# Optimization experiments

Hardware: AMD Instinct MI355X
Metric: run time of the kernel (lower is better)

## Reference

```python
import jax, jax.numpy as jnp
import numpy as np


def _conv(x, w, b, pad):
    # x: (B,C,H,W), w: (O,I,kh,kw), NCHW conv with given padding
    y = jax.lax.conv_general_dilated(x, w, window_strides=(1, 1), padding=pad,
                                     dimension_numbers=('NCHW', 'OIHW', 'NCHW'))
    return y + b[None, :, None, None]


def _frn(x, eps):
    # FilterResponseNorm: normalize by rms over spatial dims (2,3)
    nu2 = jnp.mean(x * x, axis=(2, 3), keepdims=True)
    return x * jax.lax.rsqrt(nu2 + jnp.abs(eps))


def _mish(x):
    return x * jnp.tanh(jax.nn.softplus(x))


def setup_inputs() -> dict:
    key = jax.random.key(0)
    ks = jax.random.split(key, 9)
    B, C, H, W = 4, 256, 64, 64
    C16 = C // 16
    x = jax.random.normal(ks[0], (B, C, H, W), dtype=jnp.float32)
    s = 0.05
    wq = jax.random.normal(ks[1], (C16, C, 1, 3), dtype=jnp.float32) * s
    bq = jax.random.normal(ks[2], (C16,), dtype=jnp.float32) * s
    wk = jax.random.normal(ks[3], (C16, C, 3, 1), dtype=jnp.float32) * s
    bk = jax.random.normal(ks[4], (C16,), dtype=jnp.float32) * s
    wv = jax.random.normal(ks[5], (C, C, 1, 1), dtype=jnp.float32) * s
    bv = jax.random.normal(ks[6], (C,), dtype=jnp.float32) * s
    gamma = jax.random.normal(ks[7], (1,), dtype=jnp.float32) * 0.1
    eps_q = jnp.full((1, C16, 1, 1), 1e-6, dtype=jnp.float32)
    eps_k = jnp.full((1, C16, 1, 1), 1e-6, dtype=jnp.float32)
    return {"x": x, "wq": wq, "bq": bq, "wk": wk, "bk": bk,
            "wv": wv, "bv": bv, "gamma": gamma, "eps_q": eps_q, "eps_k": eps_k}


def reference(x, wq, bq, wk, bk, wv, bv, gamma, eps_q, eps_k):
    B, C, H, W = x.shape
    N = H * W
    # query branch: Conv2d(k=(1,3), pad=(0,1)) -> FRN -> Mish
    q = _mish(_frn(_conv(x, wq, bq, [(0, 0), (1, 1)]), eps_q))  # (B,C16,H,W)
    # key branch: Conv2d(k=(3,1), pad=(1,0)) -> FRN -> Mish
    k = _mish(_frn(_conv(x, wk, bk, [(1, 1), (0, 0)]), eps_k))  # (B,C16,H,W)
    q = q.reshape(B, -1, N)  # (B,C16,N)
    k = k.reshape(B, -1, N)  # (B,C16,N)
    # affinity[b,n,m] = sum_c q[b,c,n] * k[b,c,m]; softmax over m
    affinity = jnp.einsum('bcn,bcm->bnm', q, k)
    affinity = jax.nn.softmax(affinity, axis=-1)  # (B,N,N)
    v = _conv(x, wv, bv, [(0, 0), (0, 0)]).reshape(B, C, N)  # (B,C,N)
    # weights = v @ affinity^T : weights[b,c,j] = sum_n v[b,c,n] * affinity[b,j,n]
    weights = jnp.einsum('bcn,bjn->bcj', v, affinity).reshape(B, C, H, W)
    return gamma * weights + x
```

## Files before the change

kernel.cpp:

```cpp
#include <hip/hip_runtime.h>
#include <stdint.h>

#define NB 4
#define CC 256
#define C16 16
#define HH 64
#define WW 64
#define NN 4096

typedef __attribute__((ext_vector_type(8))) short short8;
typedef __attribute__((ext_vector_type(4))) float floatx4;
typedef __attribute__((ext_vector_type(16))) float floatx16;

#if __has_builtin(__builtin_amdgcn_exp2f)
#define EXP2(x) __builtin_amdgcn_exp2f(x)
#else
#define EXP2(x) exp2f(x)
#endif

__device__ __forceinline__ unsigned short f2bf(float f) {
    union { float f; unsigned u; } v; v.f = f;
    unsigned r = v.u + 0x7fffu + ((v.u >> 16) & 1u);
    return (unsigned short)(r >> 16);
}
__device__ __forceinline__ float bf2f(unsigned short h) {
    union { unsigned u; float f; } v; v.u = (unsigned)h << 16;
    return v.f;
}


__global__ __launch_bounds__(256) void prep_kernel(
        const float* __restrict__ x, const float* __restrict__ wv,
        const float* __restrict__ wq, const float* __restrict__ wk,
        unsigned short* __restrict__ xT, unsigned short* __restrict__ wvb,
        unsigned short* __restrict__ wqkb, float* __restrict__ nu2) {
    int bid = blockIdx.x;
    if (bid < 1024) {
        __shared__ float tile_t[64][65];
        int nt = bid & 63, ct = (bid >> 6) & 3, b = bid >> 8;
        int n0 = nt * 64, c0 = ct * 64;
        int tid = threadIdx.x;
        int rg = tid >> 4, f = tid & 15;
        const float* xb = x + ((size_t)b * CC + c0) * NN + n0;
#pragma unroll
        for (int p = 0; p < 4; ++p) {
            int c = p * 16 + rg;
            float4 v = *(const float4*)(xb + (size_t)c * NN + f * 4);
            tile_t[f * 4 + 0][c] = v.x;
            tile_t[f * 4 + 1][c] = v.y;
            tile_t[f * 4 + 2][c] = v.z;
            tile_t[f * 4 + 3][c] = v.w;
        }
        __syncthreads();
        unsigned short* xtb = xT + ((size_t)b * NN + n0) * CC + c0;
#pragma unroll
        for (int p = 0; p < 4; ++p) {
            int n = p * 16 + rg;
            ushort4 st;
            st.x = f2bf(tile_t[n][f * 4 + 0]);
            st.y = f2bf(tile_t[n][f * 4 + 1]);
            st.z = f2bf(tile_t[n][f * 4 + 2]);
            st.w = f2bf(tile_t[n][f * 4 + 3]);
            *(ushort4*)(xtb + (size_t)n * CC + f * 4) = st;
        }
    } else {
        int idx = (bid - 1024) * 256 + threadIdx.x;
        if (bid == 1024 && threadIdx.x < 128) nu2[threadIdx.x] = 0.f;
        if (idx < 16384) {
            float4 v = *(const float4*)(wv + idx * 4);
            ushort4 o;
            o.x = f2bf(v.x); o.y = f2bf(v.y); o.z = f2bf(v.z); o.w = f2bf(v.w);
            *(ushort4*)(wvb + idx * 4) = o;
        } else if (idx < 16384 + 6144) {
            int base = (idx - 16384) * 4;
#pragma unroll
            for (int u = 0; u < 4; ++u) {
                int e = base + u;
                int t = e / 12288;
                int i = e - t * 12288;
                int tap = i >> 12, o = (i >> 8) & 15, c = i & 255;
                const float* src = t ? wk : wq;
                wqkb[e] = f2bf(src[o * 768 + c * 3 + tap]);
            }
        }
    }
}

__global__ __launch_bounds__(256) void conv_kernel(
        const unsigned short* __restrict__ xT, const unsigned short* __restrict__ wvb,
        const unsigned short* __restrict__ wqkb, const float* __restrict__ bv,
        const float* __restrict__ bq, const float* __restrict__ bk,
        unsigned short* __restrict__ vb, unsigned short* __restrict__ qrawh,
        unsigned short* __restrict__ krawh, float* __restrict__ nu2) {
    int bid = blockIdx.x;
    int tid = threadIdx.x;
    int wv_ = tid >> 6, lane = tid & 63;
    int q16 = lane >> 4, c16 = lane & 15;
    if (bid < 512) {
        int ntile = bid & 63, b = (bid >> 6) & 3, ch = bid >> 8;
        int n0 = ntile * 64;
        int cb = ch * 128 + wv_ * 32;
        floatx4 fzero = {0.f, 0.f, 0.f, 0.f};
        floatx4 acc[2][4];
        for (int ct = 0; ct < 2; ++ct)
            for (int nt = 0; nt < 4; ++nt) acc[ct][nt] = fzero;
        const unsigned short* xb = xT + ((size_t)b * NN + n0) * CC;
        for (int kc = 0; kc < 8; ++kc) {
            int ko = kc * 32 + q16 * 8;
            short8 a0 = *(const short8*)(wvb + (size_t)(cb + c16) * CC + ko);
            short8 a1 = *(const short8*)(wvb + (size_t)(cb + 16 + c16) * CC + ko);
            short8 bf[4];
#pragma unroll
            for (int nt = 0; nt < 4; ++nt)
                bf[nt] = *(const short8*)(xb + (size_t)(nt * 16 + c16) * CC + ko);
#pragma unroll
            for (int nt = 0; nt < 4; ++nt) {
                acc[0][nt] = __builtin_amdgcn_mfma_f32_16x16x32_bf16(bf[nt], a0, acc[0][nt], 0, 0, 0);
                acc[1][nt] = __builtin_amdgcn_mfma_f32_16x16x32_bf16(bf[nt], a1, acc[1][nt], 0, 0, 0);
            }
        }
        float bv0 = bv[cb + c16], bv1 = bv[cb + 16 + c16];
        int off = 32 * 8 * (q16 >> 1) + (q16 & 1) * 4 + c16 * 8;
#pragma unroll
        for (int ct = 0; ct < 2; ++ct) {
            float bvv = ct ? bv1 : bv0;
#pragma unroll
            for (int nt = 0; nt < 4; ++nt) {
                size_t fb = (((size_t)b * 8 + ch * 4 + wv_) * 256 + (n0 >> 4) + nt) * 512;
                ushort4 st;
                st.x = f2bf(acc[ct][nt][0] + bvv);
                st.y = f2bf(acc[ct][nt][1] + bvv);
                st.z = f2bf(acc[ct][nt][2] + bvv);
                st.w = f2bf(acc[ct][nt][3] + bvv);
                *(ushort4*)(vb + fb + off + ct * 16 * 8) = st;
            }
        }
    } else {
        int cv = bid - 512;
        int nb2 = cv & 63, b = cv >> 6;
        int nl = nb2 * 64 + wv_ * 16 + c16;
        int h = nl >> 6, w = nl & 63;
        bool vm1 = (w != 0), vp1 = (w != 63);
        bool vm64 = (h != 0), vp64 = (h != 63);
        short8 zero8 = {0, 0, 0, 0, 0, 0, 0, 0};
        floatx4 accq = {0.f, 0.f, 0.f, 0.f}, acck = {0.f, 0.f, 0.f, 0.f};
        const unsigned short* xb = xT + (size_t)b * NN * CC;
        const unsigned short* wrow = wqkb + c16 * 256;
        for (int kc = 0; kc < 8; ++kc) {
            int ko = kc * 32 + q16 * 8;
            short8 b0 = *(const short8*)(xb + (size_t)nl * CC + ko);
            short8 bm1 = vm1 ? *(const short8*)(xb + (size_t)(nl - 1) * CC + ko) : zero8;
            short8 bp1 = vp1 ? *(const short8*)(xb + (size_t)(nl + 1) * CC + ko) : zero8;
            short8 bm64 = vm64 ? *(const short8*)(xb + (size_t)(nl - 64) * CC + ko) : zero8;
            short8 bp64 = vp64 ? *(const short8*)(xb + (size_t)(nl + 64) * CC + ko) : zero8;
            short8 aq0 = *(const short8*)(wrow + 0 * 4096 + ko);
            short8 aq1 = *(const short8*)(wrow + 1 * 4096 + ko);
            short8 aq2 = *(const short8*)(wrow + 2 * 4096 + ko);
            short8 ak0 = *(const short8*)(wrow + 12288 + 0 * 4096 + ko);
            short8 ak1 = *(const short8*)(wrow + 12288 + 1 * 4096 + ko);
            short8 ak2 = *(const short8*)(wrow + 12288 + 2 * 4096 + ko);
            accq = __builtin_amdgcn_mfma_f32_16x16x32_bf16(bm1, aq0, accq, 0, 0, 0);
            accq = __builtin_amdgcn_mfma_f32_16x16x32_bf16(b0, aq1, accq, 0, 0, 0);
            accq = __builtin_amdgcn_mfma_f32_16x16x32_bf16(bp1, aq2, accq, 0, 0, 0);
            acck = __builtin_amdgcn_mfma_f32_16x16x32_bf16(bm64, ak0, acck, 0, 0, 0);
            acck = __builtin_amdgcn_mfma_f32_16x16x32_bf16(b0, ak1, acck, 0, 0, 0);
            acck = __builtin_amdgcn_mfma_f32_16x16x32_bf16(bp64, ak2, acck, 0, 0, 0);
        }
        int nst = nb2 * 64 + wv_ * 16 + q16 * 4;
        float bqv = bq[c16], bkv = bk[c16];
        ushort4 sq4, sk4;
        float ssq = 0.f, ssk = 0.f;
        {
            float vq0 = accq[0] + bqv, vq1 = accq[1] + bqv, vq2 = accq[2] + bqv, vq3 = accq[3] + bqv;
            float vk0 = acck[0] + bkv, vk1 = acck[1] + bkv, vk2 = acck[2] + bkv, vk3 = acck[3] + bkv;
            sq4.x = f2bf(vq0); sq4.y = f2bf(vq1); sq4.z = f2bf(vq2); sq4.w = f2bf(vq3);
            sk4.x = f2bf(vk0); sk4.y = f2bf(vk1); sk4.z = f2bf(vk2); sk4.w = f2bf(vk3);
            ssq = vq0 * vq0 + vq1 * vq1 + vq2 * vq2 + vq3 * vq3;
            ssk = vk0 * vk0 + vk1 * vk1 + vk2 * vk2 + vk3 * vk3;
        }
        *(ushort4*)(qrawh + (size_t)(b * C16 + c16) * NN + nst) = sq4;
        *(ushort4*)(krawh + (size_t)(b * C16 + c16) * NN + nst) = sk4;
        ssq += __shfl_xor(ssq, 16, 64);
        ssq += __shfl_xor(ssq, 32, 64);
        ssk += __shfl_xor(ssk, 16, 64);
        ssk += __shfl_xor(ssk, 32, 64);
        if (lane < 16) {
            atomicAdd(nu2 + b * C16 + lane, ssq);
            atomicAdd(nu2 + 64 + b * C16 + lane, ssk);
        }
    }
}

__global__ __launch_bounds__(256) void frn_mish_kernel(
        const unsigned short* __restrict__ qrawh, const unsigned short* __restrict__ krawh,
        const float* __restrict__ nu2, const float* __restrict__ eps_q,
        const float* __restrict__ eps_k, unsigned short* __restrict__ qb,
        unsigned short* __restrict__ kb) {
    int blk = blockIdx.x;
    int tensor = blk >> 8;
    int b = (blk >> 6) & 3;
    int nch = blk & 63;
    const unsigned short* raw = tensor ? krawh : qrawh;
    const float* eps = tensor ? eps_k : eps_q;
    unsigned short* outp = tensor ? kb : qb;
    const float* nu = nu2 + tensor * 64 + b * C16;
    float scale = tensor ? 1.0f : 1.44269504f;
    int n = nch * 64 + (threadIdx.x & 63);
    int oq = threadIdx.x >> 6;
    ushort4 pk4;
#pragma unroll
    for (int i = 0; i < 4; ++i) {
        int o = oq * 4 + i;
        float r = bf2f(raw[(size_t)(b * C16 + o) * NN + n]);
        float v = r * rsqrtf(nu[o] * (1.f / (float)NN) + fabsf(eps[o]));
        float sp = fmaxf(v, 0.f) + log1pf(expf(-fabsf(v)));
        float m = v * tanhf(sp) * scale;
        ((unsigned short*)&pk4)[i] = f2bf(m);
    }
    size_t base = ((size_t)b * 128 + (n >> 5)) * 512 + (size_t)(n & 31) * 8
                + (size_t)(oq >> 1) * 256 + (oq & 1) * 4;
    *(ushort4*)(outp + base) = pk4;
}

__device__ __forceinline__ void pack_half(
        const floatx16& sc, int h, short8* A, float* lsum) {
    unsigned pk[4];
    float ls = 0.f;
#pragma unroll
    for (int p = 0; p < 4; ++p) {
        float e0 = EXP2(sc[8 * h + 2 * p]);
        float e1 = EXP2(sc[8 * h + 2 * p + 1]);
        ls += e0 + e1;
        pk[p] = __builtin_amdgcn_perm(__float_as_uint(e1), __float_as_uint(e0), 0x07060302u);
    }
    *lsum += ls;
    asm("v_permlane32_swap_b32 %0, %1" : "+v"(pk[0]), "+v"(pk[2]));
    asm("v_permlane32_swap_b32 %0, %1" : "+v"(pk[1]), "+v"(pk[3]));
    union { unsigned u[4]; short8 s; } a;
    a.u[0] = pk[0]; a.u[1] = pk[1]; a.u[2] = pk[2]; a.u[3] = pk[3];
    *A = a.s;
}

__global__ __launch_bounds__(256, 2) void attn_kernel(
        const unsigned short* __restrict__ qb, const unsigned short* __restrict__ kb,
        const unsigned short* __restrict__ vb, const float* __restrict__ x,
        const float* __restrict__ gamma_p, float* __restrict__ out) {
    __shared__ float lpart[4][2][32];
    __shared__ float obuf[4][32][33];

    int tid = threadIdx.x;
    int wv_ = __builtin_amdgcn_readfirstlane(tid >> 6);
    int lane = tid & 63;
    int l31 = lane & 31, lh = lane >> 5;
    int id = blockIdx.x;
    int cs = id & 1, b = (id >> 1) & 3, jt = id >> 3;
    int jbase = jt * 64, cb = cs * 128;
    int lane8 = lane * 8;

    const unsigned short* qfb = qb + ((size_t)b * 128 + (jbase >> 5)) * 512 + lane8;
    const unsigned short* kfb = kb + ((size_t)b * 128 + (wv_ * 32)) * 512 + lane8;

    short8 qf0 = *(const short8*)qfb;
    short8 qf1 = *(const short8*)(qfb + 512);

    floatx16 z16 = {0,0,0,0,0,0,0,0,0,0,0,0,0,0,0,0};
    floatx16 acc0[4], acc1[4];
#pragma unroll
    for (int cg = 0; cg < 4; ++cg) { acc0[cg] = z16; acc1[cg] = z16; }
    float lsum0 = 0.f, lsum1 = 0.f;

    const unsigned short* vp0 = vb + (((size_t)b * 8 + cs * 4 + 0) * 256 + wv_ * 64) * 512 + lane8;
    const unsigned short* vp1 = vb + (((size_t)b * 8 + cs * 4 + 1) * 256 + wv_ * 64) * 512 + lane8;
    const unsigned short* vp2 = vb + (((size_t)b * 8 + cs * 4 + 2) * 256 + wv_ * 64) * 512 + lane8;
    const unsigned short* vp3 = vb + (((size_t)b * 8 + cs * 4 + 3) * 256 + wv_ * 64) * 512 + lane8;

    short8 ak = *(const short8*)kfb;
#pragma unroll 1
    for (int step = 0; step < 32; ++step) {
        short8 vf0a = *(const short8*)vp0;
        short8 vf1a = *(const short8*)vp1;
        short8 vf2a = *(const short8*)vp2;
        short8 vf3a = *(const short8*)vp3;
        short8 vf0b = *(const short8*)(vp0 + 512);
        short8 vf1b = *(const short8*)(vp1 + 512);
        short8 vf2b = *(const short8*)(vp2 + 512);
        short8 vf3b = *(const short8*)(vp3 + 512);
        floatx16 sc0 = __builtin_amdgcn_mfma_f32_32x32x16_bf16(ak, qf0, z16, 0, 0, 0);
        floatx16 sc1 = __builtin_amdgcn_mfma_f32_32x32x16_bf16(ak, qf1, z16, 0, 0, 0);
        ak = *(const short8*)(kfb + (size_t)((step + 1) & 31) * 512);
        short8 A;
        pack_half(sc0, 0, &A, &lsum0);
        __builtin_amdgcn_s_setprio(1);
        acc0[0] = __builtin_amdgcn_mfma_f32_32x32x16_bf16(A, vf0a, acc0[0], 0, 0, 0);
        acc0[1] = __builtin_amdgcn_mfma_f32_32x32x16_bf16(A, vf1a, acc0[1], 0, 0, 0);
        acc0[2] = __builtin_amdgcn_mfma_f32_32x32x16_bf16(A, vf2a, acc0[2], 0, 0, 0);
        acc0[3] = __builtin_amdgcn_mfma_f32_32x32x16_bf16(A, vf3a, acc0[3], 0, 0, 0);
        __builtin_amdgcn_s_setprio(0);
        __builtin_amdgcn_sched_barrier(0);
        pack_half(sc0, 1, &A, &lsum0);
        __builtin_amdgcn_s_setprio(1);
        acc0[0] = __builtin_amdgcn_mfma_f32_32x32x16_bf16(A, vf0b, acc0[0], 0, 0, 0);
        acc0[1] = __builtin_amdgcn_mfma_f32_32x32x16_bf16(A, vf1b, acc0[1], 0, 0, 0);
        acc0[2] = __builtin_amdgcn_mfma_f32_32x32x16_bf16(A, vf2b, acc0[2], 0, 0, 0);
        acc0[3] = __builtin_amdgcn_mfma_f32_32x32x16_bf16(A, vf3b, acc0[3], 0, 0, 0);
        __builtin_amdgcn_s_setprio(0);
        __builtin_amdgcn_sched_barrier(0);
        pack_half(sc1, 0, &A, &lsum1);
        __builtin_amdgcn_s_setprio(1);
        acc1[0] = __builtin_amdgcn_mfma_f32_32x32x16_bf16(A, vf0a, acc1[0], 0, 0, 0);
        acc1[1] = __builtin_amdgcn_mfma_f32_32x32x16_bf16(A, vf1a, acc1[1], 0, 0, 0);
        acc1[2] = __builtin_amdgcn_mfma_f32_32x32x16_bf16(A, vf2a, acc1[2], 0, 0, 0);
        acc1[3] = __builtin_amdgcn_mfma_f32_32x32x16_bf16(A, vf3a, acc1[3], 0, 0, 0);
        __builtin_amdgcn_s_setprio(0);
        __builtin_amdgcn_sched_barrier(0);
        pack_half(sc1, 1, &A, &lsum1);
        __builtin_amdgcn_s_setprio(1);
        acc1[0] = __builtin_amdgcn_mfma_f32_32x32x16_bf16(A, vf0b, acc1[0], 0, 0, 0);
        acc1[1] = __builtin_amdgcn_mfma_f32_32x32x16_bf16(A, vf1b, acc1[1], 0, 0, 0);
        acc1[2] = __builtin_amdgcn_mfma_f32_32x32x16_bf16(A, vf2b, acc1[2], 0, 0, 0);
        acc1[3] = __builtin_amdgcn_mfma_f32_32x32x16_bf16(A, vf3b, acc1[3], 0, 0, 0);
        __builtin_amdgcn_s_setprio(0);
        vp0 += 1024; vp1 += 1024; vp2 += 1024; vp3 += 1024;
    }

    lsum0 += __shfl_xor(lsum0, 32, 64);
    lsum1 += __shfl_xor(lsum1, 32, 64);
    if (lh == 0) { lpart[wv_][0][l31] = lsum0; lpart[wv_][1][l31] = lsum1; }
    __syncthreads();

    int j31 = tid & 31;
    float gamma = gamma_p[0];
    float gl0 = gamma / (lpart[0][0][j31] + lpart[1][0][j31] + lpart[2][0][j31] + lpart[3][0][j31]);
    float gl1 = gamma / (lpart[0][1][j31] + lpart[1][1][j31] + lpart[2][1][j31] + lpart[3][1][j31]);
    const float* xbb = x + (size_t)b * CC * NN;
    float* obb = out + (size_t)b * CC * NN;
    int hofs = lh * 4;
    int cgrp = tid >> 5;
#pragma unroll
    for (int jg = 0; jg < 2; ++jg) {
        float gl = jg ? gl1 : gl0;
#pragma unroll
        for (int cg = 0; cg < 4; ++cg) {
            __syncthreads();
            const floatx16& a = jg ? acc1[cg] : acc0[cg];
#pragma unroll
            for (int r = 0; r < 16; ++r) {
                int row = (r & 3) + 8 * (r >> 2) + hofs;
                obuf[wv_][row][l31] = a[r];
            }
            __syncthreads();
#pragma unroll
            for (int i = 0; i < 4; ++i) {
                int c = cgrp * 4 + i;
                float val = obuf[0][j31][c] + obuf[1][j31][c] + obuf[2][j31][c] + obuf[3][j31][c];
                size_t oidx = (size_t)(cb + cg * 32 + c) * NN + jbase + jg * 32 + j31;
                obb[oidx] = fmaf(gl, val, xbb[oidx]);
            }
        }
    }
}

extern "C" void kernel_launch(void* const* d_in, const int* in_sizes, int n_in,
                              void* d_out, int out_size, void* d_ws, size_t ws_size,
                              hipStream_t stream) {
    const float* x     = (const float*)d_in[0];
    const float* wq    = (const float*)d_in[1];
    const float* bq    = (const float*)d_in[2];
    const float* wk    = (const float*)d_in[3];
    const float* bk    = (const float*)d_in[4];
    const float* wv    = (const float*)d_in[5];
    const float* bv    = (const float*)d_in[6];
    const float* gamma = (const float*)d_in[7];
    const float* eps_q = (const float*)d_in[8];
    const float* eps_k = (const float*)d_in[9];
    float* out = (float*)d_out;

    char* ws = (char*)d_ws;
    unsigned short* qrawh = (unsigned short*)ws;
    unsigned short* krawh = (unsigned short*)(ws + (1u << 20));
    float* nu2  = (float*)(ws + (2u << 20));
    unsigned short* qb = (unsigned short*)(ws + (2u << 20) + 4096);
    unsigned short* kb = qb + (size_t)NB * NN * C16;
    unsigned short* vb = kb + (size_t)NB * NN * C16;
    unsigned short* xT = vb + (size_t)NB * CC * NN;
    unsigned short* wvb = xT + (size_t)NB * NN * CC;
    unsigned short* wqkb = wvb + (size_t)CC * CC;

    prep_kernel<<<dim3(1112), dim3(256), 0, stream>>>(x, wv, wq, wk, xT, wvb, wqkb, nu2);
    conv_kernel<<<dim3(768), dim3(256), 0, stream>>>(xT, wvb, wqkb, bv, bq, bk, vb, qrawh, krawh, nu2);
    frn_mish_kernel<<<dim3(512), dim3(256), 0, stream>>>(qrawh, krawh, nu2, eps_q, eps_k, qb, kb);
    attn_kernel<<<dim3(512), dim3(256), 0, stream>>>(qb, kb, vb, x, gamma, out);
}
```

Baseline: 163.3 us.

## Double-buffer V fragments through LDS with async global_load_lds prefetch

The V operand loads in the attention main loop no longer go straight from global memory into registers. They are now issued as asynchronous global-to-LDS loads into per-wave double buffers one step ahead, then read back from LDS after an explicit vmcnt wait. The goal is to hide global-memory latency behind the MFMA and exp work of the current step. In exchange LDS use grows to about 66 KB per block, and the output staging buffer now aliases the stage buffers. The final prefetch reads one step past the end of each V slice.

```diff
diff --git a/kernel.cpp b/kernel.cpp
--- a/kernel.cpp
+++ b/kernel.cpp
@@ -26,6 +26,12 @@
 __device__ __forceinline__ float bf2f(unsigned short h) {
     union { unsigned u; float f; } v; v.u = (unsigned)h << 16;
     return v.f;
+}
+
+__device__ __forceinline__ void gll16(const unsigned short* g, char* l) {
+    __builtin_amdgcn_global_load_lds(
+        (const __attribute__((address_space(1))) void*)g,
+        (__attribute__((address_space(3))) void*)l, 16, 0, 0);
 }
 
 
@@ -245,8 +251,9 @@
         const unsigned short* __restrict__ qb, const unsigned short* __restrict__ kb,
         const unsigned short* __restrict__ vb, const float* __restrict__ x,
         const float* __restrict__ gamma_p, float* __restrict__ out) {
-    __shared__ float lpart[4][2][32];
-    __shared__ float obuf[4][32][33];
+    __shared__ __align__(1024) char smem[66560];
+    float (*lpart)[2][32] = (float (*)[2][32])(smem + 65536);
+    float (*obuf)[32][33] = (float (*)[32][33])smem;
 
     int tid = threadIdx.x;
     int wv_ = __builtin_amdgcn_readfirstlane(tid >> 6);
@@ -256,6 +263,10 @@
     int cs = id & 1, b = (id >> 1) & 3, jt = id >> 3;
     int jbase = jt * 64, cb = cs * 128;
     int lane8 = lane * 8;
+    int lane16 = lane * 16;
+
+    char* st0 = smem + wv_ * 8192;
+    char* st1 = st0 + 32768;
 
     const unsigned short* qfb = qb + ((size_t)b * 128 + (jbase >> 5)) * 512 + lane8;
     const unsigned short* kfb = kb + ((size_t)b * 128 + (wv_ * 32)) * 512 + lane8;
@@ -274,54 +285,84 @@
     const unsigned short* vp2 = vb + (((size_t)b * 8 + cs * 4 + 2) * 256 + wv_ * 64) * 512 + lane8;
     const unsigned short* vp3 = vb + (((size_t)b * 8 + cs * 4 + 3) * 256 + wv_ * 64) * 512 + lane8;
 
-    short8 ak = *(const short8*)kfb;
+#define STAGE8(WRB) do { \
+        gll16(vp0,       (WRB) + 0 * 1024); \
+        gll16(vp1,       (WRB) + 1 * 1024); \
+        gll16(vp2,       (WRB) + 2 * 1024); \
+        gll16(vp3,       (WRB) + 3 * 1024); \
+        gll16(vp0 + 512, (WRB) + 4 * 1024); \
+        gll16(vp1 + 512, (WRB) + 5 * 1024); \
+        gll16(vp2 + 512, (WRB) + 6 * 1024); \
+        gll16(vp3 + 512, (WRB) + 7 * 1024); \
+        vp0 += 1024; vp1 += 1024; vp2 += 1024; vp3 += 1024; \
+    } while (0)
+
+    STAGE8(st0);
+    short8 ak0 = *(const short8*)kfb;
+    short8 ak1;
+    int kstep = 1;
+
+#define STEP(RDB, WRB, AKC, AKN) do { \
+        STAGE8(WRB); \
+        AKN = *(const short8*)(kfb + (size_t)(kstep & 31) * 512); ++kstep; \
+        __builtin_amdgcn_sched_barrier(0); \
+        asm volatile("s_waitcnt vmcnt(10)" ::: "memory"); \
+        __builtin_amdgcn_sched_barrier(0); \
+        short8 vf0a = *(const short8*)((RDB) + 0 * 1024 + lane16); \
+        short8 vf1a = *(const short8*)((RDB) + 1 * 1024 + lane16); \
+        short8 vf2a = *(const short8*)((RDB) + 2 * 1024 + lane16); \
+        short8 vf3a = *(const short8*)((RDB) + 3 * 1024 + lane16); \
+        short8 vf0b = *(const short8*)((RDB) + 4 * 1024 + lane16); \
+        short8 vf1b = *(const short8*)((RDB) + 5 * 1024 + lane16); \
+        short8 vf2b = *(const short8*)((RDB) + 6 * 1024 + lane16); \
+        short8 vf3b = *(const short8*)((RDB) + 7 * 1024 + lane16); \
+        floatx16 sc0 = __builtin_amdgcn_mfma_f32_32x32x16_bf16(AKC, qf0, z16, 0, 0, 0); \
+        floatx16 sc1 = __builtin_amdgcn_mfma_f32_32x32x16_bf16(AKC, qf1, z16, 0, 0, 0); \
+        short8 A; \
+        pack_half(sc0, 0, &A, &lsum0); \
+        __builtin_amdgcn_s_setprio(1); \
+        acc0[0] = __builtin_amdgcn_mfma_f32_32x32x16_bf16(A, vf0a, acc0[0], 0, 0, 0); \
+        acc0[1] = __builtin_amdgcn_mfma_f32_32x32x16_bf16(A, vf1a, acc0[1], 0, 0, 0); \
+        acc0[2] = __builtin_amdgcn_mfma_f32_32x32x16_bf16(A, vf2a, acc0[2], 0, 0, 0); \
+        acc0[3] = __builtin_amdgcn_mfma_f32_32x32x16_bf16(A, vf3a, acc0[3], 0, 0, 0); \
+        __builtin_amdgcn_s_setprio(0); \
+        __builtin_amdgcn_sched_barrier(0); \
+        pack_half(sc0, 1, &A, &lsum0); \
+        __builtin_amdgcn_s_setprio(1); \
+        acc0[0] = __builtin_amdgcn_mfma_f32_32x32x16_bf16(A, vf0b, acc0[0], 0, 0, 0); \
+        acc0[1] = __builtin_amdgcn_mfma_f32_32x32x16_bf16(A, vf1b, acc0[1], 0, 0, 0); \
+        acc0[2] = __builtin_amdgcn_mfma_f32_32x32x16_bf16(A, vf2b, acc0[2], 0, 0, 0); \
+        acc0[3] = __builtin_amdgcn_mfma_f32_32x32x16_bf16(A, vf3b, acc0[3], 0, 0, 0); \
+        __builtin_amdgcn_s_setprio(0); \
+        __builtin_amdgcn_sched_barrier(0); \
+        pack_half(sc1, 0, &A, &lsum1); \
+        __builtin_amdgcn_s_setprio(1); \
+        acc1[0] = __builtin_amdgcn_mfma_f32_32x32x16_bf16(A, vf0a, acc1[0], 0, 0, 0); \
+        acc1[1] = __builtin_amdgcn_mfma_f32_32x32x16_bf16(A, vf1a, acc1[1], 0, 0, 0); \
+        acc1[2] = __builtin_amdgcn_mfma_f32_32x32x16_bf16(A, vf2a, acc1[2], 0, 0, 0); \
+        acc1[3] = __builtin_amdgcn_mfma_f32_32x32x16_bf16(A, vf3a, acc1[3], 0, 0, 0); \
+        __builtin_amdgcn_s_setprio(0); \
+        __builtin_amdgcn_sched_barrier(0); \
+        pack_half(sc1, 1, &A, &lsum1); \
+        __builtin_amdgcn_s_setprio(1); \
+        acc1[0] = __builtin_amdgcn_mfma_f32_32x32x16_bf16(A, vf0b, acc1[0], 0, 0, 0); \
+        acc1[1] = __builtin_amdgcn_mfma_f32_32x32x16_bf16(A, vf1b, acc1[1], 0, 0, 0); \
+        acc1[2] = __builtin_amdgcn_mfma_f32_32x32x16_bf16(A, vf2b, acc1[2], 0, 0, 0); \
+        acc1[3] = __builtin_amdgcn_mfma_f32_32x32x16_bf16(A, vf3b, acc1[3], 0, 0, 0); \
+        __builtin_amdgcn_s_setprio(0); \
+    } while (0)
+
 #pragma unroll 1
-    for (int step = 0; step < 32; ++step) {
-        short8 vf0a = *(const short8*)vp0;
-        short8 vf1a = *(const short8*)vp1;
-        short8 vf2a = *(const short8*)vp2;
-        short8 vf3a = *(const short8*)vp3;
-        short8 vf0b = *(const short8*)(vp0 + 512);
-        short8 vf1b = *(const short8*)(vp1 + 512);
-        short8 vf2b = *(const short8*)(vp2 + 512);
-        short8 vf3b = *(const short8*)(vp3 + 512);
-        floatx16 sc0 = __builtin_amdgcn_mfma_f32_32x32x16_bf16(ak, qf0, z16, 0, 0, 0);
-        floatx16 sc1 = __builtin_amdgcn_mfma_f32_32x32x16_bf16(ak, qf1, z16, 0, 0, 0);
-        ak = *(const short8*)(kfb + (size_t)((step + 1) & 31) * 512);
-        short8 A;
-        pack_half(sc0, 0, &A, &lsum0);
-        __builtin_amdgcn_s_setprio(1);
-        acc0[0] = __builtin_amdgcn_mfma_f32_32x32x16_bf16(A, vf0a, acc0[0], 0, 0, 0);
-        acc0[1] = __builtin_amdgcn_mfma_f32_32x32x16_bf16(A, vf1a, acc0[1], 0, 0, 0);
-        acc0[2] = __builtin_amdgcn_mfma_f32_32x32x16_bf16(A, vf2a, acc0[2], 0, 0, 0);
-        acc0[3] = __builtin_amdgcn_mfma_f32_32x32x16_bf16(A, vf3a, acc0[3], 0, 0, 0);
-        __builtin_amdgcn_s_setprio(0);
-        __builtin_amdgcn_sched_barrier(0);
-        pack_half(sc0, 1, &A, &lsum0);
-        __builtin_amdgcn_s_setprio(1);
-        acc0[0] = __builtin_amdgcn_mfma_f32_32x32x16_bf16(A, vf0b, acc0[0], 0, 0, 0);
-        acc0[1] = __builtin_amdgcn_mfma_f32_32x32x16_bf16(A, vf1b, acc0[1], 0, 0, 0);
-        acc0[2] = __builtin_amdgcn_mfma_f32_32x32x16_bf16(A, vf2b, acc0[2], 0, 0, 0);
-        acc0[3] = __builtin_amdgcn_mfma_f32_32x32x16_bf16(A, vf3b, acc0[3], 0, 0, 0);
-        __builtin_amdgcn_s_setprio(0);
-        __builtin_amdgcn_sched_barrier(0);
-        pack_half(sc1, 0, &A, &lsum1);
-        __builtin_amdgcn_s_setprio(1);
-        acc1[0] = __builtin_amdgcn_mfma_f32_32x32x16_bf16(A, vf0a, acc1[0], 0, 0, 0);
-        acc1[1] = __builtin_amdgcn_mfma_f32_32x32x16_bf16(A, vf1a, acc1[1], 0, 0, 0);
-        acc1[2] = __builtin_amdgcn_mfma_f32_32x32x16_bf16(A, vf2a, acc1[2], 0, 0, 0);
-        acc1[3] = __builtin_amdgcn_mfma_f32_32x32x16_bf16(A, vf3a, acc1[3], 0, 0, 0);
-        __builtin_amdgcn_s_setprio(0);
-        __builtin_amdgcn_sched_barrier(0);
-        pack_half(sc1, 1, &A, &lsum1);
-        __builtin_amdgcn_s_setprio(1);
-        acc1[0] = __builtin_amdgcn_mfma_f32_32x32x16_bf16(A, vf0b, acc1[0], 0, 0, 0);
-        acc1[1] = __builtin_amdgcn_mfma_f32_32x32x16_bf16(A, vf1b, acc1[1], 0, 0, 0);
-        acc1[2] = __builtin_amdgcn_mfma_f32_32x32x16_bf16(A, vf2b, acc1[2], 0, 0, 0);
-        acc1[3] = __builtin_amdgcn_mfma_f32_32x32x16_bf16(A, vf3b, acc1[3], 0, 0, 0);
-        __builtin_amdgcn_s_setprio(0);
-        vp0 += 1024; vp1 += 1024; vp2 += 1024; vp3 += 1024;
-    }
+    for (int it = 0; it < 16; ++it) {
+        STEP(st0, st1, ak0, ak1);
+        STEP(st1, st0, ak1, ak0);
+    }
+#undef STEP
+#undef STAGE8
+
+    __builtin_amdgcn_sched_barrier(0);
+    asm volatile("s_waitcnt vmcnt(0)" ::: "memory");
+    __builtin_amdgcn_sched_barrier(0);
 
     lsum0 += __shfl_xor(lsum0, 32, 64);
     lsum1 += __shfl_xor(lsum1, 32, 64);
```

New measurement: 166.2 us. About the same (+1.8%).
